# Kernel optimization log

Measured on AMD Instinct MI355X. Metric: run time of the kernel, lower is better.

The kernel has to match this reference:

```python
import jax, jax.numpy as jnp
import numpy as np

STEPS, K, NEW_PTS, GDIM, HDIM = 10, 64, 1152, 256, 128


def setup_inputs() -> dict:
    key = jax.random.key(0)
    ks = jax.random.split(key, 24)
    def w(k, shape):
        return jax.random.normal(k, shape, dtype=jnp.float32) * 0.02
    inp = {
        'points': jax.random.normal(ks[0], (4, 4096, 3), dtype=jnp.float32),
        'gt': jax.random.normal(ks[1], (4, 4096, 3), dtype=jnp.float32),
        # PointNet encoder: 3->64->128->256 (stored [in,out])
        'enc_w1': w(ks[2], (3, 64)),   'enc_b1': jnp.zeros((64,), jnp.float32),
        'enc_w2': w(ks[3], (64, 128)), 'enc_b2': jnp.zeros((128,), jnp.float32),
        'enc_w3': w(ks[4], (128, GDIM)), 'enc_b3': jnp.zeros((GDIM,), jnp.float32),
        # Attention MLP: (3+256+128)->128->1
        'att_w1': w(ks[5], (3 + GDIM + HDIM, 128)), 'att_b1': jnp.zeros((128,), jnp.float32),
        'att_w2': w(ks[6], (128, 1)), 'att_b2': jnp.zeros((1,), jnp.float32),
        # LSTMCell: input 256+3+3=262, hidden 128, gates i,f,g,o
        'lstm_wih': w(ks[7], (GDIM + 6, 4 * HDIM)), 'lstm_whh': w(ks[8], (HDIM, 4 * HDIM)),
        'lstm_bih': jnp.zeros((4 * HDIM,), jnp.float32), 'lstm_bhh': jnp.zeros((4 * HDIM,), jnp.float32),
        # Refiner: 128->128->new_points*3
        'ref_w1': w(ks[9], (HDIM, 128)), 'ref_b1': jnp.zeros((128,), jnp.float32),
        'ref_w2': w(ks[10], (128, NEW_PTS * 3)), 'ref_b2': jnp.zeros((NEW_PTS * 3,), jnp.float32),
    }
    return inp


def _chamfer_sq(x, y):
    # x: [B,N,3], y: [B,M,3]; squared-L2 chamfer, batch-mean (pytorch3d norm=2)
    d2 = (jnp.sum(x * x, -1)[:, :, None] + jnp.sum(y * y, -1)[:, None, :]
          - 2.0 * jnp.einsum('bnd,bmd->bnm', x, y))  # [B,N,M]
    cd = jnp.mean(jnp.min(d2, axis=2), axis=1) + jnp.mean(jnp.min(d2, axis=1), axis=1)
    return jnp.mean(cd)


def _forward(points, gt, enc_w1, enc_b1, enc_w2, enc_b2, enc_w3, enc_b3,
             att_w1, att_b1, att_w2, att_b2,
             lstm_wih, lstm_whh, lstm_bih, lstm_bhh,
             ref_w1, ref_b1, ref_w2, ref_b2):
    B, N0, _ = points.shape
    h = jnp.zeros((B, HDIM), points.dtype)
    c = jnp.zeros((B, HDIM), points.dtype)
    canvas = points
    for _ in range(STEPS):
        # PointNet encoder + max-pool -> global feature [B,GDIM]
        f = jax.nn.relu(canvas @ enc_w1 + enc_b1)
        f = jax.nn.relu(f @ enc_w2 + enc_b2)
        f = f @ enc_w3 + enc_b3
        gfeat = jnp.max(f, axis=1)
        # attention-weighted centroid
        N = canvas.shape[1]
        ctx = jnp.concatenate([
            canvas,
            jnp.broadcast_to(gfeat[:, None, :], (B, N, GDIM)),
            jnp.broadcast_to(h[:, None, :], (B, N, HDIM)),
        ], axis=-1)
        scores = (jax.nn.relu(ctx @ att_w1 + att_b1) @ att_w2 + att_b2)[..., 0]  # [B,N]
        alpha = jax.nn.softmax(scores, axis=1)
        center = jnp.einsum('bn,bnd->bd', alpha, canvas)
        # brute-force KNN around center + gather
        dist = jnp.linalg.norm(canvas - center[:, None, :], axis=-1)  # [B,N]
        _, idx = jax.lax.top_k(-dist, K)  # smallest K
        patch = jnp.take_along_axis(canvas, idx[:, :, None], axis=1)  # [B,K,3]
        patch_feat = jnp.mean(patch - center[:, None, :], axis=1)  # [B,3]
        # LSTM cell (gate order i,f,g,o)
        lstm_in = jnp.concatenate([gfeat, center, patch_feat], axis=1)
        gates = lstm_in @ lstm_wih + lstm_bih + h @ lstm_whh + lstm_bhh
        gi, gf, gg, go = jnp.split(gates, 4, axis=1)
        c = jax.nn.sigmoid(gf) * c + jax.nn.sigmoid(gi) * jnp.tanh(gg)
        h = jax.nn.sigmoid(go) * jnp.tanh(c)
        # refine: generate new patch points around center
        new_pts = (jax.nn.relu(h @ ref_w1 + ref_b1) @ ref_w2 + ref_b2)
        new_pts = new_pts.reshape(B, NEW_PTS, 3) * 0.02 + center[:, None, :]
        canvas = jnp.concatenate([canvas, new_pts], axis=1)
    p_input = canvas[:, :N0, :]
    p_new = canvas[:, N0:, :]
    total_loss = 0.1 * _chamfer_sq(p_input, gt) + 1.0 * _chamfer_sq(p_new, gt)
    return total_loss


def reference(points, gt, enc_w1, enc_b1, enc_w2, enc_b2, enc_w3, enc_b3,
              att_w1, att_b1, att_w2, att_b2,
              lstm_wih, lstm_whh, lstm_bih, lstm_bhh,
              ref_w1, ref_b1, ref_w2, ref_b2):
    return _forward(points, gt, enc_w1, enc_b1, enc_w2, enc_b2, enc_w3, enc_b3,
                    att_w1, att_b1, att_w2, att_b2,
                    lstm_wih, lstm_whh, lstm_bih, lstm_bhh,
                    ref_w1, ref_b1, ref_w2, ref_b2)
```

## Files before the change

kernel.cpp:

```cpp
#include <hip/hip_runtime.h>
#include <math.h>

#define BB 4
#define N0 4096
#define NEWP 1152
#define GD 256
#define HD 128
#define KSEL 64
#define NSTEPS 10
#define NMAX (N0 + NSTEPS*NEWP)
#define NNEW (NSTEPS*NEWP)
#define F2S (BB*N0)

#define OFF_CANVAS 0
#define OFF_MINAB  (OFF_CANVAS + BB*NMAX*3)
#define OFF_MINCD  (OFF_MINAB + 2*BB*N0)
#define OFF_GMAX   (OFF_MINCD + BB*NNEW + BB*N0)
#define OFF_H      (OFF_GMAX + BB*GD)
#define OFF_C      (OFF_H + 2*BB*HD)
#define OFF_ACC    (OFF_C + 2*BB*HD)
#define OFF_CENTER (OFF_ACC + 16)
#define OFF_PART   (OFF_CENTER + 32)
#define OFF_GPART  (OFF_PART + BB*32*8)
#define OFF_F2     (OFF_GPART + 32*BB*512)
#define WS_FLOATS  (OFF_F2 + 128*F2S)

__device__ __forceinline__ unsigned enc_f(float f){
  unsigned u = __float_as_uint(f);
  return (u & 0x80000000u) ? ~u : (u | 0x80000000u);
}
__device__ __forceinline__ float dec_f(unsigned e){
  unsigned u = (e & 0x80000000u) ? (e & 0x7fffffffu) : ~e;
  return __uint_as_float(u);
}
__device__ __forceinline__ float sigm(float x){ return 1.f/(1.f+expf(-x)); }

__device__ __forceinline__ float block_sum(float v, volatile float* red){
#pragma unroll
  for (int s=32;s>0;s>>=1) v += __shfl_down(v, s, 64);
  int lane = threadIdx.x & 63, w = threadIdx.x >> 6, nw = blockDim.x >> 6;
  __syncthreads();
  if (lane==0) red[w] = v;
  __syncthreads();
  if (w==0){
    float x = (lane < nw) ? red[lane] : 0.f;
#pragma unroll
    for (int s=8;s>0;s>>=1) x += __shfl_down(x, s, 64);
    if (lane==0) red[0] = x;
  }
  __syncthreads();
  float r = red[0];
  __syncthreads();
  return r;
}
__device__ __forceinline__ float block_max(float v, volatile float* red){
#pragma unroll
  for (int s=32;s>0;s>>=1) v = fmaxf(v, __shfl_down(v, s, 64));
  int lane = threadIdx.x & 63, w = threadIdx.x >> 6, nw = blockDim.x >> 6;
  __syncthreads();
  if (lane==0) red[w] = v;
  __syncthreads();
  if (w==0){
    float x = (lane < nw) ? red[lane] : -3.4e38f;
#pragma unroll
    for (int s=8;s>0;s>>=1) x = fmaxf(x, __shfl_down(x, s, 64));
    if (lane==0) red[0] = x;
  }
  __syncthreads();
  float r = red[0];
  __syncthreads();
  return r;
}

__global__ __launch_bounds__(512) void init_kernel(
    const float* __restrict__ points,
    float* __restrict__ canvas, unsigned* __restrict__ minAB,
    unsigned* __restrict__ minCD, unsigned* __restrict__ gmax,
    float* __restrict__ h, float* __restrict__ c)
{
  int gid = blockIdx.x*512 + threadIdx.x;
  if (gid < BB*N0*3){
    int b = gid/(N0*3), r = gid - b*(N0*3);
    canvas[(size_t)b*NMAX*3 + r] = points[gid];
  }
  if (gid < 2*BB*N0) minAB[gid] = 0xFFFFFFFFu;
  if (gid < BB*NNEW + BB*N0) minCD[gid] = 0xFFFFFFFFu;
  if (gid < BB*GD) gmax[gid] = 0u;
  if (gid < 2*BB*HD){ h[gid]=0.f; c[gid]=0.f; }
}

__global__ __launch_bounds__(256) void enc12_kernel(
    const float* __restrict__ canvas, const float* __restrict__ w1,
    const float* __restrict__ b1, const float* __restrict__ w2,
    const float* __restrict__ b2, float* __restrict__ f2buf,
    int off, int M)
{
  int b = blockIdx.y;
  int jc = blockIdx.z;
  int i = blockIdx.x*256 + threadIdx.x;
  int ii = (i < M) ? i : 0;
  const float* p = canvas + (size_t)(b*NMAX + off + ii)*3;
  float p0 = p[0], p1 = p[1], p2 = p[2];
  float f1[64];
#pragma unroll
  for (int j=0;j<64;j++)
    f1[j] = fmaxf(0.f, b1[j] + p0*w1[j] + p1*w1[64+j] + p2*w1[128+j]);
  float a[16];
  const float* b2p = b2 + jc*16;
#pragma unroll
  for (int j=0;j<16;j++) a[j] = b2p[j];
#pragma unroll
  for (int k=0;k<64;k++){
    const float* wr = w2 + k*128 + jc*16;
#pragma unroll
    for (int j=0;j<16;j++) a[j] = fmaf(f1[k], wr[j], a[j]);
  }
  if (i < M){
    int base = b*N0 + i;
#pragma unroll
    for (int j=0;j<16;j++)
      f2buf[(size_t)(jc*16 + j)*F2S + base] = fmaxf(a[j], 0.f);
  }
}

__global__ __launch_bounds__(256) void enc3_kernel(
    const float* __restrict__ f2buf, const float* __restrict__ w3,
    const float* __restrict__ b3, unsigned* __restrict__ gmax, int M)
{
  int b = blockIdx.y;
  int dc = blockIdx.z;
  int i = blockIdx.x*256 + threadIdx.x;
  bool act = i < M;
  int ii = act ? i : 0;
  const float* fp = f2buf + b*N0 + ii;
  float a[16];
  const float* b3p = b3 + dc*16;
#pragma unroll
  for (int d=0;d<16;d++) a[d] = b3p[d];
  for (int k=0;k<128;k++){
    float fk = fp[(size_t)k*F2S];
    const float* wr = w3 + k*256 + dc*16;
#pragma unroll
    for (int d=0;d<16;d++) a[d] = fmaf(fk, wr[d], a[d]);
  }
#pragma unroll
  for (int d=0;d<16;d++){
    float v = act ? a[d] : -3.4e38f;
#pragma unroll
    for (int s=32;s>0;s>>=1) v = fmaxf(v, __shfl_down(v, s, 64));
    if ((threadIdx.x & 63) == 0) atomicMax(&gmax[b*GD + dc*16 + d], enc_f(v));
  }
}

__global__ __launch_bounds__(512) void sl_kernel(
    const float* __restrict__ canvas, const float* __restrict__ aw1,
    const float* __restrict__ ab1, const float* __restrict__ aw2,
    const float* __restrict__ ab2, const unsigned* __restrict__ gmax,
    const float* __restrict__ h_in,
    const float* __restrict__ wih, const float* __restrict__ whh,
    float* __restrict__ part, float* __restrict__ gpart, int N, int nch)
{
  __shared__ float sBatt[128];
  __shared__ float red[16];
  __shared__ float sV[BB][12];
  int blk = blockIdx.x;
  int tid = threadIdx.x;
  if (blk < 4*nch){
    int b = blk / nch, ch = blk - b*nch;
    if (tid < 128){
      float a = ab1[tid];
      for (int k=0;k<GD;k++) a += dec_f(gmax[b*GD+k]) * aw1[(3+k)*128 + tid];
      for (int k=0;k<HD;k++) a += h_in[b*HD+k] * aw1[(3+GD+k)*128 + tid];
      sBatt[tid] = a;
    }
    __syncthreads();
    int i = ch*512 + tid;
    bool act = i < N;
    float p0=0.f,p1=0.f,p2=0.f,s=-3.4e38f;
    if (act){
      const float* pp = canvas + (size_t)(b*NMAX + i)*3;
      p0=pp[0]; p1=pp[1]; p2=pp[2];
      s = ab2[0];
      for (int j=0;j<128;j++){
        float v = sBatt[j] + p0*aw1[j] + p1*aw1[128+j] + p2*aw1[256+j];
        s += fmaxf(v, 0.f)*aw2[j];
      }
    }
    float mb = block_max(s, red);
    float e = act ? expf(s - mb) : 0.f;
    float se = block_sum(e, red);
    float wx = block_sum(e*p0, red);
    float wy = block_sum(e*p1, red);
    float wz = block_sum(e*p2, red);
    if (tid==0){
      float* pr = part + (size_t)(b*32 + ch)*8;
      pr[0]=mb; pr[1]=se; pr[2]=wx; pr[3]=wy; pr[4]=wz;
    }
  } else {
    int cc = blk - 4*nch;
    if (tid < BB*12){
      int b = tid/12, j = tid - b*12;
      int r = cc*12 + j;
      sV[b][j] = (r < 256) ? dec_f(gmax[b*GD + r]) : h_in[b*HD + (r-256)];
    }
    __syncthreads();
    float a0=0.f,a1=0.f,a2=0.f,a3=0.f;
#pragma unroll
    for (int j=0;j<12;j++){
      int r = cc*12 + j;
      const float* wr = (r < 256) ? (wih + (size_t)r*512) : (whh + (size_t)(r-256)*512);
      float wvv = wr[tid];
      a0 += sV[0][j]*wvv; a1 += sV[1][j]*wvv;
      a2 += sV[2][j]*wvv; a3 += sV[3][j]*wvv;
    }
    float* gp = gpart + (size_t)cc*(BB*512);
    gp[0*512+tid]=a0; gp[1*512+tid]=a1; gp[2*512+tid]=a2; gp[3*512+tid]=a3;
  }
}

template<int Q>
__global__ __launch_bounds__(1024) void stepA_kernel(
    const float* __restrict__ canvas, const float* __restrict__ part,
    float* __restrict__ centerpf, int N, int nch)
{
  __shared__ float red[16];
  __shared__ float sC[3];
  __shared__ unsigned cbufA[2][16];
  __shared__ unsigned cbufB[2][16];
  __shared__ int tieCnt;
  __shared__ int tieIdx[256];

  int b = blockIdx.x;
  int tid = threadIdx.x;
  int lane = tid & 63, wid = tid >> 6;
  const float* cv = canvas + (size_t)b*NMAX*3;

  float pm=-3.4e38f, pse=0.f, pwx=0.f, pwy=0.f, pwz=0.f;
  if (tid < nch){
    const float* pp = part + (size_t)(b*32 + tid)*8;
    pm=pp[0]; pse=pp[1]; pwx=pp[2]; pwy=pp[3]; pwz=pp[4];
  }
  float M = block_max(pm, red);
  float w = (tid < nch) ? expf(pm - M) : 0.f;
  float se = block_sum(pse*w, red);
  float wx = block_sum(pwx*w, red);
  float wy = block_sum(pwy*w, red);
  float wz = block_sum(pwz*w, red);
  if (tid==0){ sC[0]=wx/se; sC[1]=wy/se; sC[2]=wz/se; }
  __syncthreads();
  float cx=sC[0], cy=sC[1], cz=sC[2];
  if (tid<3) centerpf[b*3+tid] = sC[tid];

  unsigned ur[Q];
#pragma unroll
  for (int q=0;q<Q;q++){
    ur[q] = 0xFFFFFFFFu;
    int i = tid + q*1024;
    if (i < N){
      const float* p = cv + (size_t)i*3;
      float dx=p[0]-cx, dy=p[1]-cy, dz=p[2]-cz;
      ur[q] = __float_as_uint(dx*dx + dy*dy + dz*dz);
    }
  }

  unsigned T = 0u;
  int cntBelow = 0;
  int par = 0;
  {
    unsigned cand = 1u<<30;
    unsigned tc = 0;
#pragma unroll
    for (int q=0;q<Q;q++) tc += (ur[q] < cand) ? 1u : 0u;
#pragma unroll
    for (int s=32;s>0;s>>=1) tc += __shfl_down(tc, s, 64);
    if (lane==0) cbufA[par][wid] = tc;
    __syncthreads();
    unsigned tot = 0;
#pragma unroll
    for (int i2=0;i2<16;i2++) tot += cbufA[par][i2];
    if ((int)tot < KSEL){ T = cand; cntBelow = (int)tot; }
    par ^= 1;
  }
  for (int bit=29; bit>=1; bit-=2){
    unsigned q1 = 1u<<(bit-1);
    unsigned c1 = T + q1, c2 = T + 2u*q1, c3 = T + 3u*q1;
    unsigned ta = 0, tb = 0;
#pragma unroll
    for (int q=0;q<Q;q++){
      unsigned u = ur[q];
      ta += (u < c1 ? 1u : 0u) | (u < c2 ? 0x10000u : 0u);
      tb += (u < c3 ? 1u : 0u);
    }
#pragma unroll
    for (int s=32;s>0;s>>=1){ ta += __shfl_down(ta, s, 64); tb += __shfl_down(tb, s, 64); }
    if (lane==0){ cbufA[par][wid] = ta; cbufB[par][wid] = tb; }
    __syncthreads();
    unsigned sa = 0, sb = 0;
#pragma unroll
    for (int i2=0;i2<16;i2++){ sa += cbufA[par][i2]; sb += cbufB[par][i2]; }
    int n1 = (int)(sa & 0xFFFFu), n2 = (int)(sa >> 16), n3 = (int)sb;
    if (n3 < KSEL){ T = c3; cntBelow = n3; }
    else if (n2 < KSEL){ T = c2; cntBelow = n2; }
    else if (n1 < KSEL){ T = c1; cntBelow = n1; }
    par ^= 1;
  }
  int kneed = KSEL - cntBelow;

  if (tid==0) tieCnt = 0;
  __syncthreads();
  float sx=0.f, sy=0.f, sz=0.f;
#pragma unroll
  for (int q=0;q<Q;q++){
    unsigned u = ur[q];
    if (u < T){
      const float* p = cv + (size_t)(tid + q*1024)*3;
      sx += p[0]; sy += p[1]; sz += p[2];
    } else if (u == T){
      int pos = atomicAdd(&tieCnt, 1);
      if (pos < 256) tieIdx[pos] = tid + q*1024;
    }
  }
  __syncthreads();
  sx = block_sum(sx, red);
  sy = block_sum(sy, red);
  sz = block_sum(sz, red);
  if (tid==0){
    int mm = tieCnt < 256 ? tieCnt : 256;
    for (int t=0;t<kneed;t++){
      int best=-1, bi=0x7fffffff;
      for (int q=0;q<mm;q++){ int v = tieIdx[q]; if (v < bi){ bi=v; best=q; } }
      if (best >= 0){
        tieIdx[best] = 0x7fffffff;
        const float* p = cv + (size_t)bi*3;
        sx += p[0]; sy += p[1]; sz += p[2];
      }
    }
    centerpf[16 + b*3 + 0] = sx/KSEL - cx;
    centerpf[16 + b*3 + 1] = sy/KSEL - cy;
    centerpf[16 + b*3 + 2] = sz/KSEL - cz;
  }
}

__global__ __launch_bounds__(256) void refenc12_kernel(
    float* __restrict__ canvas, const float* __restrict__ gpart,
    const float* __restrict__ centerpf,
    const float* __restrict__ c_in, float* __restrict__ c_out,
    float* __restrict__ h_out,
    const float* __restrict__ wih,
    const float* __restrict__ bih, const float* __restrict__ bhh,
    const float* __restrict__ rw1, const float* __restrict__ rb1,
    const float* __restrict__ rw2, const float* __restrict__ rb2,
    const float* __restrict__ w1, const float* __restrict__ b1,
    const float* __restrict__ w2, const float* __restrict__ b2,
    float* __restrict__ f2buf, int N)
{
  __shared__ float sG[512];
  __shared__ float sH[HD];
  __shared__ float sRf[HD];
  int b = blockIdx.y;
  int jc = blockIdx.z;
  int tid = threadIdx.x;
  float cx = centerpf[b*3+0], cy = centerpf[b*3+1], cz = centerpf[b*3+2];
  float fx = centerpf[16+b*3+0], fy = centerpf[16+b*3+1], fz = centerpf[16+b*3+2];
#pragma unroll
  for (int half=0; half<2; half++){
    int o = tid + half*256;
    float gg = bih[o] + bhh[o];
    for (int cc=0; cc<32; cc++) gg += gpart[(size_t)cc*(BB*512) + b*512 + o];
    gg += cx*wih[(size_t)256*512+o] + cy*wih[(size_t)257*512+o] + cz*wih[(size_t)258*512+o];
    gg += fx*wih[(size_t)259*512+o] + fy*wih[(size_t)260*512+o] + fz*wih[(size_t)261*512+o];
    sG[o] = gg;
  }
  __syncthreads();
  if (tid < HD){
    float gi=sG[tid], gf=sG[128+tid], gg2=sG[256+tid], go=sG[384+tid];
    float cn = sigm(gf)*c_in[b*HD+tid] + sigm(gi)*tanhf(gg2);
    float hn = sigm(go)*tanhf(cn);
    sH[tid] = hn;
    if (blockIdx.x==0 && jc==0){ c_out[b*HD+tid]=cn; h_out[b*HD+tid]=hn; }
  }
  __syncthreads();
  if (tid < HD){
    float a = rb1[tid];
    for (int k=0;k<HD;k++) a += sH[k]*rw1[k*HD + tid];
    sRf[tid] = fmaxf(a, 0.f);
  }
  __syncthreads();
  int i = blockIdx.x*256 + tid;
  bool act = i < NEWP;
  int ic = act ? i : 0;
  float a0 = rb2[3*ic], a1 = rb2[3*ic+1], a2 = rb2[3*ic+2];
  for (int k=0;k<HD;k++){
    const float* wv = rw2 + (size_t)k*(NEWP*3) + 3*ic;
    float hk = sRf[k];
    a0 = fmaf(hk, wv[0], a0); a1 = fmaf(hk, wv[1], a1); a2 = fmaf(hk, wv[2], a2);
  }
  float p0 = fmaf(a0, 0.02f, cx), p1 = fmaf(a1, 0.02f, cy), p2 = fmaf(a2, 0.02f, cz);
  if (act && jc==0){
    float* cp = canvas + ((size_t)b*NMAX + N + i)*3;
    cp[0]=p0; cp[1]=p1; cp[2]=p2;
  }
  float f1[64];
#pragma unroll
  for (int j=0;j<64;j++)
    f1[j] = fmaxf(0.f, b1[j] + p0*w1[j] + p1*w1[64+j] + p2*w1[128+j]);
  float a[16];
  const float* b2p = b2 + jc*16;
#pragma unroll
  for (int j=0;j<16;j++) a[j] = b2p[j];
#pragma unroll
  for (int k=0;k<64;k++){
    const float* wr = w2 + k*128 + jc*16;
#pragma unroll
    for (int j=0;j<16;j++) a[j] = fmaf(f1[k], wr[j], a[j]);
  }
  if (act){
    int base = b*N0 + i;
#pragma unroll
    for (int j=0;j<16;j++)
      f2buf[(size_t)(jc*16 + j)*F2S + base] = fmaxf(a[j], 0.f);
  }
}

__global__ __launch_bounds__(512) void chamfer_kernel(
    const float* __restrict__ canvas, const float* __restrict__ gt,
    unsigned* __restrict__ minAB, unsigned* __restrict__ minCD)
{
  __shared__ float sy0[1024], sy1[1024], sy2[1024], sny[1024];
  int id = blockIdx.x;
  int dir, rem;
  if (id < 32){ dir=0; rem=id; }
  else if (id < 64){ dir=1; rem=id-32; }
  else if (id < 160){ dir=2; rem=id-64; }
  else { dir=3; rem=id-160; }
  int b, xb, yb;
  if (dir < 2){ b = rem>>3; int l = rem&7; xb = l>>2; yb = l&3; }
  else if (dir == 2){ b = rem/24; int l = rem%24; xb = l>>2; yb = l&3; }
  else { b = rem/24; int l = rem%24; xb = l/12; yb = l%12; }

  int Nx, Ny; const float* X; const float* Y; unsigned* mp;
  if (dir==0){      Nx=N0;   Ny=N0;   X=canvas+(size_t)b*NMAX*3;       Y=gt+(size_t)b*N0*3;            mp=minAB + b*N0; }
  else if (dir==1){ Nx=N0;   Ny=N0;   X=gt+(size_t)b*N0*3;             Y=canvas+(size_t)b*NMAX*3;      mp=minAB + BB*N0 + b*N0; }
  else if (dir==2){ Nx=NNEW; Ny=N0;   X=canvas+((size_t)b*NMAX+N0)*3;  Y=gt+(size_t)b*N0*3;            mp=minCD + b*NNEW; }
  else {            Nx=N0;   Ny=NNEW; X=gt+(size_t)b*N0*3;             Y=canvas+((size_t)b*NMAX+N0)*3; mp=minCD + BB*NNEW + b*N0; }

  int xbase = xb*2048;
  int ybase = yb*1024;
  int tn = min(1024, Ny - ybase);
  int tid = threadIdx.x;
  for (int t=tid; t<tn; t+=512){
    const float* yp = Y + (size_t)(ybase+t)*3;
    float y0=yp[0], y1=yp[1], y2=yp[2];
    sy0[t]=-2.f*y0; sy1[t]=-2.f*y1; sy2[t]=-2.f*y2; sny[t]=y0*y0+y1*y1+y2*y2;
  }
  __syncthreads();

  float X0[4],X1[4],X2[4],NXr[4],MN[4]; int XI[4]; bool VA[4];
#pragma unroll
  for (int q=0;q<4;q++){
    int x = xbase + q*512 + tid;
    VA[q] = x < Nx;
    int xc = VA[q] ? x : 0;
    const float* xp = X + (size_t)xc*3;
    X0[q]=xp[0]; X1[q]=xp[1]; X2[q]=xp[2];
    NXr[q] = X0[q]*X0[q] + X1[q]*X1[q] + X2[q]*X2[q];
    MN[q] = 3.4e38f; XI[q] = xc;
  }
  const float4* v0 = (const float4*)sy0;
  const float4* v1 = (const float4*)sy1;
  const float4* v2 = (const float4*)sy2;
  const float4* vn = (const float4*)sny;
  int j4n = tn >> 2;
  for (int j=0;j<j4n;j++){
    float4 a0 = v0[j], a1 = v1[j], a2 = v2[j], an = vn[j];
#pragma unroll
    for (int e=0;e<4;e++){
      float y0 = ((const float*)&a0)[e];
      float y1 = ((const float*)&a1)[e];
      float y2 = ((const float*)&a2)[e];
      float ny = ((const float*)&an)[e];
#pragma unroll
      for (int q=0;q<4;q++){
        float d = fmaf(X0[q], y0, fmaf(X1[q], y1, fmaf(X2[q], y2, ny)));
        MN[q] = fminf(MN[q], d);
      }
    }
  }
  for (int j=j4n*4; j<tn; j++){
    float y0=sy0[j], y1=sy1[j], y2=sy2[j], ny=sny[j];
#pragma unroll
    for (int q=0;q<4;q++){
      float d = fmaf(X0[q], y0, fmaf(X1[q], y1, fmaf(X2[q], y2, ny)));
      MN[q] = fminf(MN[q], d);
    }
  }
#pragma unroll
  for (int q=0;q<4;q++)
    if (VA[q]) atomicMin(&mp[XI[q]], enc_f(MN[q] + NXr[q]));
}

__global__ __launch_bounds__(256) void chamfer_reduce_kernel(
    const unsigned* __restrict__ minAB, const unsigned* __restrict__ minCD,
    float* __restrict__ acc)
{
  __shared__ float red[16];
  int s = blockIdx.x, dir = s>>2, b = s&3;
  const unsigned* mp; int len;
  if (dir==0){      mp=minAB + b*N0;            len=N0; }
  else if (dir==1){ mp=minAB + BB*N0 + b*N0;    len=N0; }
  else if (dir==2){ mp=minCD + b*NNEW;          len=NNEW; }
  else {            mp=minCD + BB*NNEW + b*N0;  len=N0; }
  float v = 0.f;
  for (int i=threadIdx.x;i<len;i+=256) v += dec_f(mp[i]);
  v = block_sum(v, red);
  if (threadIdx.x==0) acc[s] = v;
}

__global__ void finish_kernel(const float* __restrict__ acc, float* __restrict__ out)
{
  if (threadIdx.x == 0 && blockIdx.x == 0){
    float cd1 = 0.f, cd2 = 0.f;
    for (int b=0;b<BB;b++) cd1 += acc[b]/(float)N0 + acc[4+b]/(float)N0;
    for (int b=0;b<BB;b++) cd2 += acc[8+b]/(float)NNEW + acc[12+b]/(float)N0;
    out[0] = 0.1f*(cd1/BB) + 1.0f*(cd2/BB);
  }
}

extern "C" void kernel_launch(void* const* d_in, const int* in_sizes, int n_in,
                              void* d_out, int out_size, void* d_ws, size_t ws_size,
                              hipStream_t stream) {
  (void)in_sizes; (void)n_in; (void)out_size; (void)ws_size;
  const float* points   = (const float*)d_in[0];
  const float* gt       = (const float*)d_in[1];
  const float* enc_w1   = (const float*)d_in[2];
  const float* enc_b1   = (const float*)d_in[3];
  const float* enc_w2   = (const float*)d_in[4];
  const float* enc_b2   = (const float*)d_in[5];
  const float* enc_w3   = (const float*)d_in[6];
  const float* enc_b3   = (const float*)d_in[7];
  const float* att_w1   = (const float*)d_in[8];
  const float* att_b1   = (const float*)d_in[9];
  const float* att_w2   = (const float*)d_in[10];
  const float* att_b2   = (const float*)d_in[11];
  const float* lstm_wih = (const float*)d_in[12];
  const float* lstm_whh = (const float*)d_in[13];
  const float* lstm_bih = (const float*)d_in[14];
  const float* lstm_bhh = (const float*)d_in[15];
  const float* ref_w1   = (const float*)d_in[16];
  const float* ref_b1   = (const float*)d_in[17];
  const float* ref_w2   = (const float*)d_in[18];
  const float* ref_b2   = (const float*)d_in[19];
  float* out = (float*)d_out;

  float* ws       = (float*)d_ws;
  float* canvas   = ws + OFF_CANVAS;
  unsigned* minAB = (unsigned*)(ws + OFF_MINAB);
  unsigned* minCD = (unsigned*)(ws + OFF_MINCD);
  unsigned* gmaxp = (unsigned*)(ws + OFF_GMAX);
  float* hb       = ws + OFF_H;
  float* cb       = ws + OFF_C;
  float* acc      = ws + OFF_ACC;
  float* centerb  = ws + OFF_CENTER;
  float* partb    = ws + OFF_PART;
  float* gpartb   = ws + OFF_GPART;
  float* f2buf    = ws + OFF_F2;

  init_kernel<<<dim3(128), 512, 0, stream>>>(points, canvas, minAB, minCD, gmaxp, hb, cb);
  enc12_kernel<<<dim3(16, BB, 8), 256, 0, stream>>>(canvas, enc_w1, enc_b1, enc_w2, enc_b2, f2buf, 0, N0);
  enc3_kernel<<<dim3(16, BB, 16), 256, 0, stream>>>(f2buf, enc_w3, enc_b3, gmaxp, N0);

  for (int t=0; t<NSTEPS; t++){
    int N   = N0 + t*NEWP;
    int nch = (N + 511) >> 9;
    float* h_in  = hb + (t&1)*BB*HD;
    float* h_out = hb + ((t+1)&1)*BB*HD;
    float* c_in  = cb + (t&1)*BB*HD;
    float* c_out = cb + ((t+1)&1)*BB*HD;
    sl_kernel<<<dim3(4*nch + 32), 512, 0, stream>>>(canvas, att_w1, att_b1, att_w2, att_b2,
                                                    gmaxp, h_in, lstm_wih, lstm_whh,
                                                    partb, gpartb, N, nch);
    if      (N <= 4096)  stepA_kernel<4> <<<dim3(BB), 1024, 0, stream>>>(canvas, partb, centerb, N, nch);
    else if (N <= 8192)  stepA_kernel<8> <<<dim3(BB), 1024, 0, stream>>>(canvas, partb, centerb, N, nch);
    else if (N <= 12288) stepA_kernel<12><<<dim3(BB), 1024, 0, stream>>>(canvas, partb, centerb, N, nch);
    else                 stepA_kernel<16><<<dim3(BB), 1024, 0, stream>>>(canvas, partb, centerb, N, nch);
    refenc12_kernel<<<dim3(5, BB, 8), 256, 0, stream>>>(canvas, gpartb, centerb,
                                                        c_in, c_out, h_out,
                                                        lstm_wih, lstm_bih, lstm_bhh,
                                                        ref_w1, ref_b1, ref_w2, ref_b2,
                                                        enc_w1, enc_b1, enc_w2, enc_b2,
                                                        f2buf, N);
    if (t < NSTEPS-1){
      enc3_kernel<<<dim3(5, BB, 16), 256, 0, stream>>>(f2buf, enc_w3, enc_b3, gmaxp, NEWP);
    }
  }

  chamfer_kernel<<<dim3(256), 512, 0, stream>>>(canvas, gt, minAB, minCD);
  chamfer_reduce_kernel<<<dim3(16), 256, 0, stream>>>(minAB, minCD, acc);
  finish_kernel<<<1, 64, 0, stream>>>(acc, out);
}
```

Baseline: 1.035 ms.

## Parallelize attention bias, cache points in stepA, and split chamfer work finer

The attention-bias precompute in sl_kernel is spread across all 512 threads as four partial sums, replacing the former 128-thread serial loop over 384 inputs. stepA now loads each point's coordinates into registers once and reuses them, instead of reading global memory twice. The chamfer kernel halves the points per thread (2 instead of 4) and doubles the grid to 512 blocks so more CUs are busy, with an early exit for out-of-range tiles. Several unroll pragmas are added to inner loops. The costs are more atomicMin traffic, more shared memory in sl_kernel, and extra register pressure in stepA.

Result: slower. 1.168 ms (+12.8%).

```diff
diff --git a/kernel.cpp b/kernel.cpp
--- a/kernel.cpp
+++ b/kernel.cpp
@@ -161,18 +161,28 @@
     float* __restrict__ part, float* __restrict__ gpart, int N, int nch)
 {
   __shared__ float sBatt[128];
+  __shared__ float sPart[4][128];
   __shared__ float red[16];
   __shared__ float sV[BB][12];
   int blk = blockIdx.x;
   int tid = threadIdx.x;
   if (blk < 4*nch){
     int b = blk / nch, ch = blk - b*nch;
-    if (tid < 128){
-      float a = ab1[tid];
-      for (int k=0;k<GD;k++) a += dec_f(gmax[b*GD+k]) * aw1[(3+k)*128 + tid];
-      for (int k=0;k<HD;k++) a += h_in[b*HD+k] * aw1[(3+GD+k)*128 + tid];
-      sBatt[tid] = a;
-    }
+    {
+      int j = tid & 127, kr = tid >> 7;
+      float a = (kr==0) ? ab1[j] : 0.f;
+      int r0 = kr*96;
+#pragma unroll 4
+      for (int m=0;m<96;m++){
+        int r = r0 + m;
+        float v = (r < 256) ? dec_f(gmax[b*GD + r]) : h_in[b*HD + (r-256)];
+        a = fmaf(v, aw1[(3+r)*128 + j], a);
+      }
+      sPart[kr][j] = a;
+    }
+    __syncthreads();
+    if (tid < 128)
+      sBatt[tid] = sPart[0][tid] + sPart[1][tid] + sPart[2][tid] + sPart[3][tid];
     __syncthreads();
     int i = ch*512 + tid;
     bool act = i < N;
@@ -181,6 +191,7 @@
       const float* pp = canvas + (size_t)(b*NMAX + i)*3;
       p0=pp[0]; p1=pp[1]; p2=pp[2];
       s = ab2[0];
+#pragma unroll 4
       for (int j=0;j<128;j++){
         float v = sBatt[j] + p0*aw1[j] + p1*aw1[128+j] + p2*aw1[256+j];
         s += fmaxf(v, 0.f)*aw2[j];
@@ -235,6 +246,15 @@
   int lane = tid & 63, wid = tid >> 6;
   const float* cv = canvas + (size_t)b*NMAX*3;
 
+  float px[Q], py[Q], pz[Q];
+#pragma unroll
+  for (int q=0;q<Q;q++){
+    int i = tid + q*1024;
+    int ic = (i < N) ? i : 0;
+    const float* p = cv + (size_t)ic*3;
+    px[q]=p[0]; py[q]=p[1]; pz[q]=p[2];
+  }
+
   float pm=-3.4e38f, pse=0.f, pwx=0.f, pwy=0.f, pwz=0.f;
   if (tid < nch){
     const float* pp = part + (size_t)(b*32 + tid)*8;
@@ -257,8 +277,7 @@
     ur[q] = 0xFFFFFFFFu;
     int i = tid + q*1024;
     if (i < N){
-      const float* p = cv + (size_t)i*3;
-      float dx=p[0]-cx, dy=p[1]-cy, dz=p[2]-cz;
+      float dx=px[q]-cx, dy=py[q]-cy, dz=pz[q]-cz;
       ur[q] = __float_as_uint(dx*dx + dy*dy + dz*dz);
     }
   }
@@ -313,8 +332,7 @@
   for (int q=0;q<Q;q++){
     unsigned u = ur[q];
     if (u < T){
-      const float* p = cv + (size_t)(tid + q*1024)*3;
-      sx += p[0]; sy += p[1]; sz += p[2];
+      sx += px[q]; sy += py[q]; sz += pz[q];
     } else if (u == T){
       int pos = atomicAdd(&tieCnt, 1);
       if (pos < 256) tieIdx[pos] = tid + q*1024;
@@ -366,6 +384,7 @@
   for (int half=0; half<2; half++){
     int o = tid + half*256;
     float gg = bih[o] + bhh[o];
+#pragma unroll 8
     for (int cc=0; cc<32; cc++) gg += gpart[(size_t)cc*(BB*512) + b*512 + o];
     gg += cx*wih[(size_t)256*512+o] + cy*wih[(size_t)257*512+o] + cz*wih[(size_t)258*512+o];
     gg += fx*wih[(size_t)259*512+o] + fy*wih[(size_t)260*512+o] + fz*wih[(size_t)261*512+o];
@@ -382,6 +401,7 @@
   __syncthreads();
   if (tid < HD){
     float a = rb1[tid];
+#pragma unroll 4
     for (int k=0;k<HD;k++) a += sH[k]*rw1[k*HD + tid];
     sRf[tid] = fmaxf(a, 0.f);
   }
@@ -390,6 +410,7 @@
   bool act = i < NEWP;
   int ic = act ? i : 0;
   float a0 = rb2[3*ic], a1 = rb2[3*ic+1], a2 = rb2[3*ic+2];
+#pragma unroll 4
   for (int k=0;k<HD;k++){
     const float* wv = rw2 + (size_t)k*(NEWP*3) + 3*ic;
     float hk = sRf[k];
@@ -429,14 +450,14 @@
   __shared__ float sy0[1024], sy1[1024], sy2[1024], sny[1024];
   int id = blockIdx.x;
   int dir, rem;
-  if (id < 32){ dir=0; rem=id; }
-  else if (id < 64){ dir=1; rem=id-32; }
-  else if (id < 160){ dir=2; rem=id-64; }
-  else { dir=3; rem=id-160; }
+  if (id < 64){ dir=0; rem=id; }
+  else if (id < 128){ dir=1; rem=id-64; }
+  else if (id < 320){ dir=2; rem=id-128; }
+  else { dir=3; rem=id-320; }
   int b, xb, yb;
-  if (dir < 2){ b = rem>>3; int l = rem&7; xb = l>>2; yb = l&3; }
-  else if (dir == 2){ b = rem/24; int l = rem%24; xb = l>>2; yb = l&3; }
-  else { b = rem/24; int l = rem%24; xb = l/12; yb = l%12; }
+  if (dir < 2){ b = rem>>4; int l = rem&15; xb = l>>2; yb = l&3; }
+  else if (dir == 2){ b = rem/48; int l = rem%48; xb = l>>2; yb = l&3; }
+  else { b = rem/48; int l = rem%48; xb = l/12; yb = l%12; }
 
   int Nx, Ny; const float* X; const float* Y; unsigned* mp;
   if (dir==0){      Nx=N0;   Ny=N0;   X=canvas+(size_t)b*NMAX*3;       Y=gt+(size_t)b*N0*3;            mp=minAB + b*N0; }
@@ -444,8 +465,9 @@
   else if (dir==2){ Nx=NNEW; Ny=N0;   X=canvas+((size_t)b*NMAX+N0)*3;  Y=gt+(size_t)b*N0*3;            mp=minCD + b*NNEW; }
   else {            Nx=N0;   Ny=NNEW; X=gt+(size_t)b*N0*3;             Y=canvas+((size_t)b*NMAX+N0)*3; mp=minCD + BB*NNEW + b*N0; }
 
-  int xbase = xb*2048;
+  int xbase = xb*1024;
   int ybase = yb*1024;
+  if (xbase >= Nx) return;
   int tn = min(1024, Ny - ybase);
   int tid = threadIdx.x;
   for (int t=tid; t<tn; t+=512){
@@ -455,9 +477,9 @@
   }
   __syncthreads();
 
-  float X0[4],X1[4],X2[4],NXr[4],MN[4]; int XI[4]; bool VA[4];
-#pragma unroll
-  for (int q=0;q<4;q++){
+  float X0[2],X1[2],X2[2],NXr[2],MN[2]; int XI[2]; bool VA[2];
+#pragma unroll
+  for (int q=0;q<2;q++){
     int x = xbase + q*512 + tid;
     VA[q] = x < Nx;
     int xc = VA[q] ? x : 0;
@@ -480,7 +502,7 @@
       float y2 = ((const float*)&a2)[e];
       float ny = ((const float*)&an)[e];
 #pragma unroll
-      for (int q=0;q<4;q++){
+      for (int q=0;q<2;q++){
         float d = fmaf(X0[q], y0, fmaf(X1[q], y1, fmaf(X2[q], y2, ny)));
         MN[q] = fminf(MN[q], d);
       }
@@ -489,13 +511,13 @@
   for (int j=j4n*4; j<tn; j++){
     float y0=sy0[j], y1=sy1[j], y2=sy2[j], ny=sny[j];
 #pragma unroll
-    for (int q=0;q<4;q++){
+    for (int q=0;q<2;q++){
       float d = fmaf(X0[q], y0, fmaf(X1[q], y1, fmaf(X2[q], y2, ny)));
       MN[q] = fminf(MN[q], d);
     }
   }
 #pragma unroll
-  for (int q=0;q<4;q++)
+  for (int q=0;q<2;q++)
     if (VA[q]) atomicMin(&mp[XI[q]], enc_f(MN[q] + NXr[q]));
 }
 
@@ -594,7 +616,7 @@
     }
   }
 
-  chamfer_kernel<<<dim3(256), 512, 0, stream>>>(canvas, gt, minAB, minCD);
+  chamfer_kernel<<<dim3(512), 512, 0, stream>>>(canvas, gt, minAB, minCD);
   chamfer_reduce_kernel<<<dim3(16), 256, 0, stream>>>(minAB, minCD, acc);
   finish_kernel<<<1, 64, 0, stream>>>(acc, out);
 }
```
